# Kernel tuning notes

Hardware: AMD Instinct MI355X
Metric: run time of the kernel (lower is better)

## Reference

```python
import jax, jax.numpy as jnp
import numpy as np

B, C_CLS, D_WORD, J = 1024, 80, 300, 8000
IMG_CH = 2048

def setup_inputs() -> dict:
    key = jax.random.key(0)
    ks = jax.random.split(key, 9)
    return {
        'feature': jax.random.normal(ks[0], (B, IMG_CH), jnp.float32),
        'inp': jax.random.normal(ks[1], (1, C_CLS, D_WORD), jnp.float32),
        'A': jax.random.uniform(ks[2], (C_CLS, C_CLS), jnp.float32),
        'W_gc1': jax.random.normal(ks[3], (D_WORD, 1024), jnp.float32) * (1.0 / np.sqrt(1024)),
        'W_gc2': jax.random.normal(ks[4], (1024, 2048), jnp.float32) * (1.0 / np.sqrt(2048)),
        'W_img': jax.random.normal(ks[5], (J, IMG_CH), jnp.float32) * 0.02,
        'b_img': jax.random.normal(ks[6], (J,), jnp.float32) * 0.02,
        'W_cls': jax.random.normal(ks[7], (J, 2048), jnp.float32) * 0.02,
        'b_cls': jax.random.normal(ks[8], (J,), jnp.float32) * 0.02,
    }

def _gen_adj(A):
    # torch: D = A.sum(1)**-0.5; adj = (A @ diag(D)).T @ diag(D) = D[:,None]*A.T*D[None,:]
    D = jnp.power(jnp.sum(A, axis=1), -0.5)
    return D[:, None] * A.T * D[None, :]

def reference(feature, inp, A, W_gc1, W_gc2, W_img, b_img, W_cls, b_cls):
    inp0 = inp[0]                                   # [C, 300]
    adj = jax.lax.stop_gradient(_gen_adj(A))        # [C, C], .detach() in torch
    x = adj @ (inp0 @ W_gc1)                        # gc1: [C, 1024]
    x = jax.nn.leaky_relu(x, negative_slope=0.2)
    x = adj @ (x @ W_gc2)                           # gc2: [C, 2048]
    # MFB bilinear pooling (is_usemfb=True, is_hash=False -> out_in_tmp=1, eval-mode dropout=identity)
    # original: out[b,c] = sum_j (Linear_img(feature[b])[j] * Linear_cls(x_col_c)[j])
    img_proj = feature @ W_img.T + b_img            # [B, J]
    cls_proj = x @ W_cls.T + b_cls                  # [C, J]
    x_out = img_proj @ cls_proj.T                   # [B, C]
    return x_out
```

## Files before the change

kernel.cpp:

```cpp
#include <hip/hip_runtime.h>
#include <hip/hip_bf16.h>


typedef __bf16 bf16_t;
typedef __bf16 bf16x8 __attribute__((ext_vector_type(8)));
typedef float f32x4 __attribute__((ext_vector_type(4)));

#define MFMA16(a, b, c) __builtin_amdgcn_mfma_f32_16x16x32_bf16((a), (b), (c), 0, 0, 0)

#define GLOAD_LDS16(g, l)                                     \
  __builtin_amdgcn_global_load_lds(                           \
      (const __attribute__((address_space(1))) void*)(g),     \
      (__attribute__((address_space(3))) void*)(l), 16, 0, 0)

#define PIN()                                   \
  do {                                          \
    asm volatile("" ::: "memory");              \
    __builtin_amdgcn_sched_barrier(0);          \
  } while (0)

#define BARRIER()                               \
  do {                                          \
    PIN();                                      \
    __builtin_amdgcn_s_barrier();               \
    PIN();                                      \
  } while (0)

__device__ inline bf16x8 cvt8(float4 a, float4 b) {
  bf16x8 v;
  v[0] = (bf16_t)a.x; v[1] = (bf16_t)a.y; v[2] = (bf16_t)a.z; v[3] = (bf16_t)a.w;
  v[4] = (bf16_t)b.x; v[5] = (bf16_t)b.y; v[6] = (bf16_t)b.z; v[7] = (bf16_t)b.w;
  return v;
}

__global__ void k_adj(const float* __restrict__ A, float* __restrict__ adj) {
  __shared__ float Dv[80];
  int tid = threadIdx.x;
  if (tid < 80) {
    float s = 0.f;
    #pragma unroll 4
    for (int j = 0; j < 80; ++j) s += A[tid * 80 + j];
    Dv[tid] = rsqrtf(s);
  }
  __syncthreads();
  for (int idx = tid; idx < 6400; idx += blockDim.x) {
    int i = idx / 80, j = idx % 80;
    adj[idx] = Dv[i] * Dv[j] * A[j * 80 + i];
  }
}

__global__ void k_cvt0(const float* __restrict__ inp0, bf16_t* __restrict__ x0b) {
  int idx = blockIdx.x * blockDim.x + threadIdx.x;
  if (idx < 30720) {
    int c = idx / 384, k = idx % 384;
    x0b[idx] = (k < 300) ? (bf16_t)inp0[c * 300 + k] : (bf16_t)0.f;
  }
}

__global__ __launch_bounds__(256) void k_gc1m(
    const bf16_t* __restrict__ x0b, const float* __restrict__ Wgc1,
    float* __restrict__ t1) {
  int tid = threadIdx.x;
  int w = tid >> 6, l = tid & 63;
  int ln = l & 15, q = l >> 4;
  int n0 = blockIdx.x * 16;

  __shared__ float red[4][80][16];
  f32x4 acc[5] = {};
  for (int ks = 0; ks < 3; ++ks) {
    int kq = w * 96 + ks * 32 + q * 8;
    bf16x8 bfrag;
    #pragma unroll
    for (int jj = 0; jj < 8; ++jj) {
      int k = kq + jj;
      int kc = k < 300 ? k : 299;
      float wv = Wgc1[kc * 1024 + n0 + ln];
      bfrag[jj] = (bf16_t)(k < 300 ? wv : 0.f);
    }
    #pragma unroll
    for (int mt = 0; mt < 5; ++mt) {
      bf16x8 afrag = *(const bf16x8*)(x0b + (size_t)(mt * 16 + ln) * 384 + kq);
      acc[mt] = MFMA16(afrag, bfrag, acc[mt]);
    }
  }
  #pragma unroll
  for (int mt = 0; mt < 5; ++mt)
    #pragma unroll
    for (int reg = 0; reg < 4; ++reg)
      red[w][mt * 16 + q * 4 + reg][ln] = acc[mt][reg];
  __syncthreads();
  for (int o = tid; o < 1280; o += 256) {
    int c = o >> 4, nn = o & 15;
    t1[c * 1024 + n0 + nn] = red[0][c][nn] + red[1][c][nn] + red[2][c][nn] + red[3][c][nn];
  }
}

__global__ void k_adjmul_leaky(const float* __restrict__ adj, const float* __restrict__ t1,
                               bf16_t* __restrict__ x1b) {
  int idx = blockIdx.x * blockDim.x + threadIdx.x;
  int c = idx >> 10, n = idx & 1023;
  const float* ar = adj + c * 80;
  float acc = 0.f;
  #pragma unroll 4
  for (int cc = 0; cc < 80; ++cc) acc += ar[cc] * t1[cc * 1024 + n];
  x1b[idx] = (bf16_t)(acc > 0.f ? acc : 0.2f * acc);
}

__global__ __launch_bounds__(256) void k_gc2m(
    const bf16_t* __restrict__ x1b, const float* __restrict__ Wgc2,
    float* __restrict__ t2) {
  int tid = threadIdx.x;
  int w = tid >> 6, l = tid & 63;
  int ln = l & 15, q = l >> 4;
  int nc = blockIdx.x & 31, kc = blockIdx.x >> 5;

  __shared__ float BsF[2 * 2048];
  auto stage = [&](int b, int k0) {
    #pragma unroll
    for (int it = 0; it < 2; ++it) {
      int slot = tid + it * 256;
      int kr = slot >> 4, nq = slot & 15;
      const float* src = Wgc2 + (size_t)(k0 + kr) * 2048 + nc * 64 + nq * 4;
      float* dst = BsF + b * 2048 + slot * 4;
      GLOAD_LDS16(src, dst);
    }
  };

  int kb = kc * 64;
  bf16x8 a0[5], a1[5];
  #pragma unroll
  for (int mt = 0; mt < 5; ++mt)
    a0[mt] = *(const bf16x8*)(x1b + (size_t)(mt * 16 + ln) * 1024 + kb + q * 8);
  PIN();
  stage(0, kb);
  PIN();
  stage(1, kb + 32);
  PIN();
  #pragma unroll
  for (int mt = 0; mt < 5; ++mt)
    a1[mt] = *(const bf16x8*)(x1b + (size_t)(mt * 16 + ln) * 1024 + kb + 32 + q * 8);
  PIN();

  f32x4 acc[5] = {};
  asm volatile("s_waitcnt vmcnt(7)" ::: "memory");
  BARRIER();
  {
    bf16x8 bfrag;
    #pragma unroll
    for (int jj = 0; jj < 8; ++jj) bfrag[jj] = (bf16_t)BsF[(q * 8 + jj) * 64 + w * 16 + ln];
    #pragma unroll
    for (int mt = 0; mt < 5; ++mt) acc[mt] = MFMA16(a0[mt], bfrag, acc[mt]);
  }
  asm volatile("s_waitcnt vmcnt(5)" ::: "memory");
  BARRIER();
  {
    bf16x8 bfrag;
    #pragma unroll
    for (int jj = 0; jj < 8; ++jj)
      bfrag[jj] = (bf16_t)BsF[2048 + (q * 8 + jj) * 64 + w * 16 + ln];
    #pragma unroll
    for (int mt = 0; mt < 5; ++mt) acc[mt] = MFMA16(a1[mt], bfrag, acc[mt]);
  }

  #pragma unroll
  for (int mt = 0; mt < 5; ++mt)
    #pragma unroll
    for (int reg = 0; reg < 4; ++reg)
      atomicAdd(&t2[(size_t)(mt * 16 + q * 4 + reg) * 2048 + nc * 64 + w * 16 + ln],
                acc[mt][reg]);
}

__global__ void k_adjmul_bf16(const float* __restrict__ adj, const float* __restrict__ t2,
                              bf16_t* __restrict__ x2) {
  int idx = blockIdx.x * blockDim.x + threadIdx.x;
  int c = idx >> 11, n = idx & 2047;
  const float* ar = adj + c * 80;
  float acc = 0.f;
  #pragma unroll 4
  for (int cc = 0; cc < 80; ++cc) acc += ar[cc] * t2[cc * 2048 + n];
  x2[idx] = (bf16_t)acc;
}

__global__ __launch_bounds__(256) void k_clsproj(
    const float* __restrict__ Wcls, const float* __restrict__ bcls,
    const float* __restrict__ bimg, const bf16_t* __restrict__ x2,
    bf16_t* __restrict__ P, float* __restrict__ r) {
  int tid = threadIdx.x;
  int w = tid >> 6, l = tid & 63;
  int ln = l & 15, q = l >> 4;
  int j0 = blockIdx.x * 16;
  size_t jrow = (size_t)(j0 + ln) * 2048;

  __shared__ float red[4][80][16];
  __shared__ float rloc[80];
  if (tid < 80) rloc[tid] = 0.f;

  f32x4 acc[5] = {};
  int kbase = w * 512 + q * 8;
  for (int ks = 0; ks < 16; ++ks) {
    int kq = kbase + ks * 32;
    const float4* bp = (const float4*)(Wcls + jrow + kq);
    float4 b0 = bp[0], b1 = bp[1];
    bf16x8 bfrag = cvt8(b0, b1);
    #pragma unroll
    for (int mt = 0; mt < 5; ++mt) {
      bf16x8 afrag = *(const bf16x8*)(x2 + (size_t)(mt * 16 + ln) * 2048 + kq);
      acc[mt] = MFMA16(afrag, bfrag, acc[mt]);
    }
  }
  #pragma unroll
  for (int mt = 0; mt < 5; ++mt)
    #pragma unroll
    for (int reg = 0; reg < 4; ++reg)
      red[w][mt * 16 + q * 4 + reg][ln] = acc[mt][reg];
  __syncthreads();

  for (int o = tid; o < 1280; o += 256) {
    int c = o >> 4, jj = o & 15;
    float v = red[0][c][jj] + red[1][c][jj] + red[2][c][jj] + red[3][c][jj] + bcls[j0 + jj];
    P[(size_t)c * 8000 + j0 + jj] = (bf16_t)v;
    atomicAdd(&rloc[c], bimg[j0 + jj] * v);
  }
  __syncthreads();
  if (tid < 80) atomicAdd(&r[tid], rloc[tid]);
}

__global__ __launch_bounds__(256) void k_hmat(
    const float* __restrict__ Wimg, const bf16_t* __restrict__ P, float* __restrict__ H) {
  int tid = threadIdx.x;
  int w = tid >> 6, l = tid & 63;
  int ln = l & 15, q = l >> 4;
  int nc = blockIdx.x & 31, jc = blockIdx.x >> 5;
  int jbase = jc * 320;

  __shared__ float BsF[3 * 2048];

  auto stage = [&](int b, int j0) {
    #pragma unroll
    for (int it = 0; it < 2; ++it) {
      int slot = tid + it * 256;
      int jr = slot >> 4, nq = slot & 15;
      const float* src = Wimg + (size_t)(j0 + jr) * 2048 + nc * 64 + nq * 4;
      float* dst = BsF + b * 2048 + slot * 4;
      GLOAD_LDS16(src, dst);
    }
  };
  auto loadA = [&](bf16x8* a, int j0) {
    #pragma unroll
    for (int mt = 0; mt < 5; ++mt)
      a[mt] = *(const bf16x8*)(P + (size_t)(mt * 16 + ln) * 8000 + j0 + q * 8);
  };

  f32x4 acc[5] = {};
  bf16x8 aCur[5], aNxt[5];

  loadA(aCur, jbase);
  PIN();
  stage(0, jbase);
  PIN();
  stage(1, jbase + 32);
  PIN();

  #pragma unroll
  for (int s = 0; s < 10; ++s) {
    if (s < 9) {
      loadA(aNxt, jbase + (s + 1) * 32);
      PIN();
    }
    if (s < 8) {
      stage((s + 2) % 3, jbase + (s + 2) * 32);
      PIN();
    }
    if (s == 0)      asm volatile("s_waitcnt vmcnt(9)"  ::: "memory");
    else if (s < 8)  asm volatile("s_waitcnt vmcnt(14)" ::: "memory");
    else if (s == 8) asm volatile("s_waitcnt vmcnt(12)" ::: "memory");
    else             asm volatile("s_waitcnt vmcnt(5)"  ::: "memory");
    BARRIER();
    const float* Bc = BsF + (s % 3) * 2048;
    bf16x8 bfrag;
    #pragma unroll
    for (int jj = 0; jj < 8; ++jj) bfrag[jj] = (bf16_t)Bc[(q * 8 + jj) * 64 + w * 16 + ln];
    #pragma unroll
    for (int mt = 0; mt < 5; ++mt) acc[mt] = MFMA16(aCur[mt], bfrag, acc[mt]);
    BARRIER();
    if (s < 9) {
      #pragma unroll
      for (int mt = 0; mt < 5; ++mt) aCur[mt] = aNxt[mt];
    }
  }

  #pragma unroll
  for (int mt = 0; mt < 5; ++mt)
    #pragma unroll
    for (int reg = 0; reg < 4; ++reg)
      atomicAdd(&H[(size_t)(mt * 16 + q * 4 + reg) * 2048 + nc * 64 + w * 16 + ln],
                acc[mt][reg]);
}

__global__ __launch_bounds__(256) void k_out(
    const float* __restrict__ feat, const float* __restrict__ H,
    const float* __restrict__ r, float* __restrict__ out) {
  int tid = threadIdx.x;
  int w = tid >> 6, l = tid & 63;
  int ln = l & 15, q = l >> 4;
  int mg = blockIdx.x & 15, kc = blockIdx.x >> 4;
  int m0 = mg * 64 + w * 16;
  size_t frow = (size_t)(m0 + ln) * 2048;

  f32x4 acc[5] = {};
  int kbase = kc * 64 + q * 8;
  #pragma unroll
  for (int ks = 0; ks < 2; ++ks) {
    int kq = kbase + ks * 32;
    const float4* ap = (const float4*)(feat + frow + kq);
    bf16x8 afrag = cvt8(ap[0], ap[1]);
    #pragma unroll
    for (int nt = 0; nt < 5; ++nt) {
      const float4* hp = (const float4*)(H + (size_t)(nt * 16 + ln) * 2048 + kq);
      bf16x8 bfrag = cvt8(hp[0], hp[1]);
      acc[nt] = MFMA16(afrag, bfrag, acc[nt]);
    }
  }
  #pragma unroll
  for (int nt = 0; nt < 5; ++nt)
    #pragma unroll
    for (int reg = 0; reg < 4; ++reg) {
      int b = m0 + q * 4 + reg;
      int c = nt * 16 + ln;
      float v = acc[nt][reg];
      if (kc == 0) v += r[c];
      atomicAdd(&out[b * 80 + c], v);
    }
}

extern "C" void kernel_launch(void* const* d_in, const int* in_sizes, int n_in,
                              void* d_out, int out_size, void* d_ws, size_t ws_size,
                              hipStream_t stream) {
  const float* feature = (const float*)d_in[0];
  const float* inp     = (const float*)d_in[1];
  const float* A       = (const float*)d_in[2];
  const float* Wgc1    = (const float*)d_in[3];
  const float* Wgc2    = (const float*)d_in[4];
  const float* Wimg    = (const float*)d_in[5];
  const float* bimg    = (const float*)d_in[6];
  const float* Wcls    = (const float*)d_in[7];
  const float* bcls    = (const float*)d_in[8];
  float* out = (float*)d_out;

  char* ws = (char*)d_ws;
  float*  adj = (float*)(ws + 0);
  float*  t1  = (float*)(ws + 25600);
  bf16_t* x1b = (bf16_t*)(ws + 353280);
  float*  t2  = (float*)(ws + 517120);
  bf16_t* x2  = (bf16_t*)(ws + 1172480);
  bf16_t* P   = (bf16_t*)(ws + 1500160);
  float*  H   = (float*)(ws + 2780160);
  float*  r   = (float*)(ws + 3435520);
  bf16_t* x0b = (bf16_t*)(ws + 3435840);

  hipMemsetAsync(t2, 0, 80 * 2048 * 4, stream);
  hipMemsetAsync(H, 0, 80 * 2048 * 4, stream);
  hipMemsetAsync(r, 0, 80 * 4, stream);
  hipMemsetAsync(out, 0, 1024 * 80 * 4, stream);

  k_adj<<<1, 128, 0, stream>>>(A, adj);
  k_cvt0<<<120, 256, 0, stream>>>(inp, x0b);
  k_gc1m<<<64, 256, 0, stream>>>(x0b, Wgc1, t1);
  k_adjmul_leaky<<<320, 256, 0, stream>>>(adj, t1, x1b);
  k_gc2m<<<512, 256, 0, stream>>>(x1b, Wgc2, t2);
  k_adjmul_bf16<<<640, 256, 0, stream>>>(adj, t2, x2);
  k_clsproj<<<500, 256, 0, stream>>>(Wcls, bcls, bimg, x2, P, r);
  k_hmat<<<800, 256, 0, stream>>>(Wimg, P, H);
  k_out<<<512, 256, 0, stream>>>(feature, H, r, out);
}
```

Before: 278.6 us.

## Give each wave private W_img tiles in k_hmat and drop block barriers

k_hmat now assigns each wave its own 32-column slice of W_img with a private triple-buffered LDS region. This removes the block-wide barriers and replaces them with per-wave vmcnt waits. Each wave computes two 16-wide N tiles, so every P fragment load feeds twice as many MFMAs, and the grid is halved to 400 blocks. The trade-off is fewer blocks for occupancy and more accumulator registers per thread.

Result: faster. 271.8 us (-2.4%).

```diff
diff --git a/kernel.cpp b/kernel.cpp
--- a/kernel.cpp
+++ b/kernel.cpp
@@ -230,18 +230,19 @@
   int tid = threadIdx.x;
   int w = tid >> 6, l = tid & 63;
   int ln = l & 15, q = l >> 4;
-  int nc = blockIdx.x & 31, jc = blockIdx.x >> 5;
+  int jc = blockIdx.x >> 4, ncg = blockIdx.x & 15;
   int jbase = jc * 320;
-
-  __shared__ float BsF[3 * 2048];
-
-  auto stage = [&](int b, int j0) {
-    #pragma unroll
-    for (int it = 0; it < 2; ++it) {
-      int slot = tid + it * 256;
-      int jr = slot >> 4, nq = slot & 15;
-      const float* src = Wimg + (size_t)(j0 + jr) * 2048 + nc * 64 + nq * 4;
-      float* dst = BsF + b * 2048 + slot * 4;
+  int n0 = (ncg * 4 + w) * 32;
+
+  __shared__ float Bs[4 * 3 * 1024];
+  float* Bw = Bs + w * 3072;
+
+  auto stage = [&](int buf, int jt) {
+    #pragma unroll
+    for (int it = 0; it < 4; ++it) {
+      int row = it * 8 + (l >> 3);
+      const float* src = Wimg + (size_t)(jt + row) * 2048 + n0 + (l & 7) * 4;
+      float* dst = Bw + buf * 1024 + it * 256 + l * 4;
       GLOAD_LDS16(src, dst);
     }
   };
@@ -251,7 +252,7 @@
       a[mt] = *(const bf16x8*)(P + (size_t)(mt * 16 + ln) * 8000 + j0 + q * 8);
   };
 
-  f32x4 acc[5] = {};
+  f32x4 acc[5][2] = {};
   bf16x8 aCur[5], aNxt[5];
 
   loadA(aCur, jbase);
@@ -271,18 +272,23 @@
       stage((s + 2) % 3, jbase + (s + 2) * 32);
       PIN();
     }
-    if (s == 0)      asm volatile("s_waitcnt vmcnt(9)"  ::: "memory");
-    else if (s < 8)  asm volatile("s_waitcnt vmcnt(14)" ::: "memory");
-    else if (s == 8) asm volatile("s_waitcnt vmcnt(12)" ::: "memory");
+    if (s < 8)       asm volatile("s_waitcnt vmcnt(13)" ::: "memory");
+    else if (s == 8) asm volatile("s_waitcnt vmcnt(9)"  ::: "memory");
     else             asm volatile("s_waitcnt vmcnt(5)"  ::: "memory");
-    BARRIER();
-    const float* Bc = BsF + (s % 3) * 2048;
-    bf16x8 bfrag;
-    #pragma unroll
-    for (int jj = 0; jj < 8; ++jj) bfrag[jj] = (bf16_t)Bc[(q * 8 + jj) * 64 + w * 16 + ln];
-    #pragma unroll
-    for (int mt = 0; mt < 5; ++mt) acc[mt] = MFMA16(aCur[mt], bfrag, acc[mt]);
-    BARRIER();
+    PIN();
+    const float* Bc = Bw + (s % 3) * 1024;
+    bf16x8 bfrag[2];
+    #pragma unroll
+    for (int nt = 0; nt < 2; ++nt)
+      #pragma unroll
+      for (int jj = 0; jj < 8; ++jj)
+        bfrag[nt][jj] = (bf16_t)Bc[(q * 8 + jj) * 32 + nt * 16 + ln];
+    #pragma unroll
+    for (int mt = 0; mt < 5; ++mt)
+      #pragma unroll
+      for (int nt = 0; nt < 2; ++nt)
+        acc[mt][nt] = MFMA16(aCur[mt], bfrag[nt], acc[mt][nt]);
+    PIN();
     if (s < 9) {
       #pragma unroll
       for (int mt = 0; mt < 5; ++mt) aCur[mt] = aNxt[mt];
@@ -292,9 +298,11 @@
   #pragma unroll
   for (int mt = 0; mt < 5; ++mt)
     #pragma unroll
-    for (int reg = 0; reg < 4; ++reg)
-      atomicAdd(&H[(size_t)(mt * 16 + q * 4 + reg) * 2048 + nc * 64 + w * 16 + ln],
-                acc[mt][reg]);
+    for (int nt = 0; nt < 2; ++nt)
+      #pragma unroll
+      for (int reg = 0; reg < 4; ++reg)
+        atomicAdd(&H[(size_t)(mt * 16 + q * 4 + reg) * 2048 + n0 + nt * 16 + ln],
+                  acc[mt][nt][reg]);
 }
 
 __global__ __launch_bounds__(256) void k_out(
@@ -370,6 +378,6 @@
   k_gc2m<<<512, 256, 0, stream>>>(x1b, Wgc2, t2);
   k_adjmul_bf16<<<640, 256, 0, stream>>>(adj, t2, x2);
   k_clsproj<<<500, 256, 0, stream>>>(Wcls, bcls, bimg, x2, P, r);
-  k_hmat<<<800, 256, 0, stream>>>(Wimg, P, H);
+  k_hmat<<<400, 256, 0, stream>>>(Wimg, P, H);
   k_out<<<512, 256, 0, stream>>>(feature, H, r, out);
 }
```
